# Kernel optimization log

Measured on AMD Instinct MI355X. Metric: run time of the kernel, lower is better.

Reference implementation:

```python
import jax, jax.numpy as jnp
import numpy as np

D_MODEL = 1024
NUM_HEAD = 16
D_HEAD = 64
EPS = 1e-06


def setup_inputs() -> dict:
    key = jax.random.key(0)
    ks = jax.random.split(key, 16)
    d, h = D_MODEL, 4 * D_MODEL
    s = 1.0 / np.sqrt(d)
    inp = {
        "x": jax.random.normal(ks[0], (8, 1024, d), dtype=jnp.float32),
        # LayerNorm params
        "alpha1": jnp.ones((d,), jnp.float32),
        "beta1": jnp.zeros((d,), jnp.float32),
        "alpha2": jnp.ones((d,), jnp.float32),
        "beta2": jnp.zeros((d,), jnp.float32),
        # attention projections (weights stored as [in, out])
        "w_q": jax.random.normal(ks[1], (d, d), jnp.float32) * s,
        "b_q": jnp.zeros((d,), jnp.float32),
        "w_k": jax.random.normal(ks[2], (d, d), jnp.float32) * s,
        "b_k": jnp.zeros((d,), jnp.float32),
        "w_v": jax.random.normal(ks[3], (d, d), jnp.float32) * s,
        "b_v": jnp.zeros((d,), jnp.float32),
        "w_o": jax.random.normal(ks[4], (d, d), jnp.float32) * s,
        "b_o": jnp.zeros((d,), jnp.float32),
        # MLP
        "w1": jax.random.normal(ks[5], (d, h), jnp.float32) * s,
        "b1": jnp.zeros((h,), jnp.float32),
        "w2": jax.random.normal(ks[6], (h, d), jnp.float32) * (1.0 / np.sqrt(h)),
        "b2": jnp.zeros((d,), jnp.float32),
    }
    return inp


def _layer_norm(x, alpha, beta):
    mu = jnp.mean(x, axis=-1, keepdims=True)
    # torch .var() defaults to unbiased (ddof=1) — replicate exactly
    var = jnp.var(x, axis=-1, keepdims=True, ddof=1)
    return (x - mu) / jnp.sqrt(var + EPS) * alpha + beta


def _mha(x, w_q, b_q, w_k, b_k, w_v, b_v, w_o, b_o):
    b, p, _ = x.shape
    q = (x @ w_q + b_q).reshape(b, p, NUM_HEAD, D_HEAD).transpose(0, 2, 1, 3)
    k = (x @ w_k + b_k).reshape(b, p, NUM_HEAD, D_HEAD).transpose(0, 2, 1, 3)
    v = (x @ w_v + b_v).reshape(b, p, NUM_HEAD, D_HEAD).transpose(0, 2, 1, 3)
    scores = jnp.einsum("bhqd,bhkd->bhqk", q, k) / np.sqrt(D_HEAD).astype(np.float32)
    attn = jax.nn.softmax(scores, axis=-1)
    out = jnp.einsum("bhqk,bhkd->bhqd", attn, v)
    out = out.transpose(0, 2, 1, 3).reshape(b, p, NUM_HEAD * D_HEAD)
    return out @ w_o + b_o


def reference(x, alpha1, beta1, alpha2, beta2,
              w_q, b_q, w_k, b_k, w_v, b_v, w_o, b_o,
              w1, b1, w2, b2):
    # eval mode: Dropout is identity
    x = x + _mha(_layer_norm(x, alpha1, beta1), w_q, b_q, w_k, b_k, w_v, b_v, w_o, b_o)
    h = _layer_norm(x, alpha2, beta2)
    h = jax.nn.gelu(h @ w1 + b1, approximate=False)  # nn.GELU default: exact erf
    h = h @ w2 + b2
    return x + h
```

## Files before the change

### kernel.cpp

```cpp
#include <hip/hip_runtime.h>
#include <stdint.h>

typedef float f32x4 __attribute__((ext_vector_type(4)));
typedef short s16x8 __attribute__((ext_vector_type(8)));
typedef short s16x4 __attribute__((ext_vector_type(4)));
typedef unsigned int u32x4 __attribute__((ext_vector_type(4)));

#define M_TOTAL 8192
#define DM 1024
#define HID 4096
#define SEQ 1024
#define NH 16
#define DH 64

#define BAR() __builtin_amdgcn_s_barrier()
#define LGKM0() do { asm volatile("s_waitcnt lgkmcnt(0)" ::: "memory"); __builtin_amdgcn_sched_barrier(0); } while (0)
#define VMCNT8() do { asm volatile("s_waitcnt vmcnt(8)" ::: "memory"); __builtin_amdgcn_sched_barrier(0); } while (0)
#define VMCNT0() do { asm volatile("s_waitcnt vmcnt(0)" ::: "memory"); __builtin_amdgcn_sched_barrier(0); } while (0)
#define MFMA16 __builtin_amdgcn_mfma_f32_16x16x32_bf16

__device__ __forceinline__ unsigned short f2bf(float f) {
  unsigned int u = __float_as_uint(f);
  u = (u + 0x7fffu + ((u >> 16) & 1u)) >> 16;
  return (unsigned short)u;
}

__device__ __forceinline__ void gload16(const void* g, void* l) {
  __builtin_amdgcn_global_load_lds((__attribute__((address_space(1))) void*)g,
                                   (__attribute__((address_space(3))) void*)l,
                                   16, 0, 0);
}

__device__ __forceinline__ float erf_fast(float z) {
  const float az = fabsf(z);
  const float tt = 1.0f / fmaf(0.3275911f, az, 1.0f);
  float poly = fmaf(1.061405429f, tt, -1.453152027f);
  poly = fmaf(poly, tt, 1.421413741f);
  poly = fmaf(poly, tt, -0.284496736f);
  poly = fmaf(poly, tt, 0.254829592f);
  poly *= tt;
  const float e = __expf(-az * az);
  const float r = 1.0f - poly * e;
  return (z < 0.f) ? -r : r;
}

__global__ void tcast(const float* __restrict__ W, unsigned short* __restrict__ WT,
                      int K, int N) {
  __shared__ float tile[32][33];
  const int bn = blockIdx.x, bk = blockIdx.y;
  const int tx = threadIdx.x, ty = threadIdx.y;
#pragma unroll
  for (int i = 0; i < 32; i += 8)
    tile[ty + i][tx] = W[(size_t)(bk * 32 + ty + i) * N + bn * 32 + tx];
  __syncthreads();
#pragma unroll
  for (int i = 0; i < 32; i += 8)
    WT[(size_t)(bn * 32 + ty + i) * K + bk * 32 + tx] = f2bf(tile[tx][ty + i]);
}

__global__ __launch_bounds__(256)
void vtrans(const unsigned short* __restrict__ V, unsigned short* __restrict__ VT) {
  __shared__ unsigned short tile[64][65];
  const int bh = blockIdx.y, s0 = blockIdx.x * 64;
  const int t = threadIdx.x;
  const int sr = t >> 3, c0 = (t & 7) * 8;
#pragma unroll
  for (int it = 0; it < 2; ++it) {
    const int s = it * 32 + sr;
    const s16x8 v = *(const s16x8*)(V + ((size_t)bh * SEQ + s0 + s) * DH + c0);
#pragma unroll
    for (int i = 0; i < 8; ++i) tile[c0 + i][s] = (unsigned short)v[i];
  }
  __syncthreads();
#pragma unroll
  for (int it = 0; it < 2; ++it) {
    const int d = it * 32 + sr;
    s16x8 o;
#pragma unroll
    for (int i = 0; i < 8; ++i) o[i] = (short)tile[d][c0 + i];
    *(s16x8*)(VT + ((size_t)bh * DH + d) * SEQ + s0 + c0) = o;
  }
}

__global__ __launch_bounds__(256)
void ln_kernel(const float* __restrict__ x, const float* __restrict__ alpha,
               const float* __restrict__ beta, unsigned short* __restrict__ out) {
  const int row = blockIdx.x;
  const int t = threadIdx.x;
  const int w = t >> 6, lane = t & 63;
  const float4 v = ((const float4*)(x + (size_t)row * DM))[t];

  float s = v.x + v.y + v.z + v.w;
#pragma unroll
  for (int off = 32; off; off >>= 1) s += __shfl_xor(s, off, 64);
  __shared__ float red1[4];
  __shared__ float red2[4];
  if (lane == 0) red1[w] = s;
  __syncthreads();
  const float mu = (red1[0] + red1[1] + red1[2] + red1[3]) * (1.f / 1024.f);

  const float dx = v.x - mu, dy = v.y - mu, dz = v.z - mu, dw = v.w - mu;
  float sq = dx * dx + dy * dy + dz * dz + dw * dw;
#pragma unroll
  for (int off = 32; off; off >>= 1) sq += __shfl_xor(sq, off, 64);
  if (lane == 0) red2[w] = sq;
  __syncthreads();
  const float var = (red2[0] + red2[1] + red2[2] + red2[3]) * (1.f / 1023.f);
  const float rstd = rsqrtf(var + 1e-6f);

  const float4 a = ((const float4*)alpha)[t];
  const float4 b = ((const float4*)beta)[t];
  s16x4 o;
  o[0] = (short)f2bf(dx * rstd * a.x + b.x);
  o[1] = (short)f2bf(dy * rstd * a.y + b.y);
  o[2] = (short)f2bf(dz * rstd * a.z + b.z);
  o[3] = (short)f2bf(dw * rstd * a.w + b.w);
  *(s16x4*)(out + (size_t)row * DM + 4 * t) = o;
}

template <int MODE>
__device__ __forceinline__ void epi_store(int m, int n, float v, int Nout,
                                          unsigned short* __restrict__ obf, float* of,
                                          const float* res,
                                          const float* __restrict__ bias0,
                                          const float* __restrict__ bias1,
                                          const float* __restrict__ bias2) {
  if (MODE == 0) {
    const int which = n >> 10, nn = n & 1023;
    const float* bp = (which == 0) ? bias0 : ((which == 1) ? bias1 : bias2);
    v += bp[nn];
    const int b = m >> 10, s = m & 1023, h = nn >> 6, d = nn & 63;
    obf[(size_t)which * (M_TOTAL * DM) +
        (((size_t)(b * NH + h) * SEQ + s) * DH + d)] = f2bf(v);
  } else if (MODE == 1) {
    v += bias0[n] + res[(size_t)m * Nout + n];
    of[(size_t)m * Nout + n] = v;
  } else {
    v += bias0[n];
    const float gv = 0.5f * v * (1.0f + erf_fast(v * 0.70710678118654752f));
    obf[(size_t)m * Nout + n] = f2bf(gv);
  }
}

template <int MODE>
__global__ __launch_bounds__(256, 2)
void gemmk(const unsigned short* __restrict__ A, const unsigned short* __restrict__ B,
           int K, int Nout,
           unsigned short* __restrict__ obf, float* of, const float* res,
           const float* __restrict__ bias0, const float* __restrict__ bias1,
           const float* __restrict__ bias2) {
  __shared__ __attribute__((aligned(16))) unsigned short sA[2][128 * 64];
  __shared__ __attribute__((aligned(16))) unsigned short sB[2][128 * 64];
  const int t = threadIdx.x;
  const int lane = t & 63, wid = t >> 6;
  const int g = lane >> 4, r = lane & 15;
  const int wm = wid >> 1, wn = wid & 1;

  int bid = blockIdx.y * gridDim.x + blockIdx.x;
  const int nwg = gridDim.x * gridDim.y;
  bid = (bid & 7) * (nwg >> 3) + (bid >> 3);
  const int by = bid & 63;
  const int bx = bid >> 6;
  const int m0 = by * 128, n0 = bx * 128;

  const unsigned short* Ab = A + (size_t)m0 * K;
  const unsigned short* Bb = B + (size_t)n0 * K;

  const int rb = r & 7;
  const int slot0 = (g ^ rb) * 16;
  const int slot1 = ((4 + g) ^ rb) * 16;

  f32x4 acc[4][4];
#pragma unroll
  for (int i = 0; i < 4; ++i)
#pragma unroll
    for (int j = 0; j < 4; ++j) acc[i][j] = (f32x4){0.f, 0.f, 0.f, 0.f};

  auto stage = [&](int buf, int kt) {
#pragma unroll
    for (int s2 = 0; s2 < 4; ++s2) {
      const int f = s2 * 256 + t;
      const int row = f >> 3, c = f & 7;
      const int u = c ^ (row & 7);
      gload16(Ab + (size_t)row * K + kt * 64 + u * 8, &sA[buf][(size_t)row * 64 + c * 8]);
      gload16(Bb + (size_t)row * K + kt * 64 + u * 8, &sB[buf][(size_t)row * 64 + c * 8]);
    }
  };

  const int NT = K >> 6;
  stage(0, 0);
  stage(1, (NT > 1) ? 1 : 0);
  VMCNT8();
  BAR();

  for (int tt = 0; tt < NT; ++tt) {
    const int cur = tt & 1;
    const char* sAc = (const char*)&sA[cur][0];
    const char* sBc = (const char*)&sB[cur][0];

    s16x8 av[4][2], bv[4][2];
#pragma unroll
    for (int i = 0; i < 4; ++i) {
      const int rbyte = (wm * 64 + i * 16 + r) * 128;
      av[i][0] = *(const s16x8*)(sAc + rbyte + slot0);
      av[i][1] = *(const s16x8*)(sAc + rbyte + slot1);
    }
#pragma unroll
    for (int n = 0; n < 4; ++n) {
      const int rbyte = (wn * 64 + n * 16 + r) * 128;
      bv[n][0] = *(const s16x8*)(sBc + rbyte + slot0);
      bv[n][1] = *(const s16x8*)(sBc + rbyte + slot1);
    }
    LGKM0();
    __builtin_amdgcn_s_setprio(1);
#pragma unroll
    for (int i = 0; i < 4; ++i)
#pragma unroll
      for (int n = 0; n < 4; ++n) {
        acc[i][n] = MFMA16(av[i][0], bv[n][0], acc[i][n], 0, 0, 0);
        acc[i][n] = MFMA16(av[i][1], bv[n][1], acc[i][n], 0, 0, 0);
      }
    __builtin_amdgcn_s_setprio(0);

    BAR();
    const int tp2 = (tt + 2 < NT) ? tt + 2 : NT - 1;
    stage(cur, tp2);
    VMCNT8();
    BAR();
  }

  VMCNT0();

#pragma unroll
  for (int i = 0; i < 4; ++i)
#pragma unroll
    for (int j = 0; j < 4; ++j) {
      const int m = m0 + wm * 64 + i * 16 + 4 * g + j;
#pragma unroll
      for (int nf = 0; nf < 4; ++nf) {
        const int n = n0 + wn * 64 + nf * 16 + r;
        epi_store<MODE>(m, n, acc[i][nf][j], Nout, obf, of, res, bias0, bias1, bias2);
      }
    }
}

__global__ __launch_bounds__(256)
void attn_kernel(const unsigned short* __restrict__ QKV,
                 const unsigned short* __restrict__ VT,
                 unsigned short* __restrict__ O) {
  const unsigned short* Qg = QKV;
  const unsigned short* Kg = QKV + (size_t)M_TOTAL * DM;
  const int bh = blockIdx.y;
  const int q0 = blockIdx.x * 64;
  const int t = threadIdx.x, w = t >> 6, lane = t & 63;
  const int g = lane >> 4, r = lane & 15;
  const unsigned short* Qb = Qg + (size_t)bh * SEQ * DH;
  const unsigned short* Kb = Kg + (size_t)bh * SEQ * DH;
  const unsigned short* VTb = VT + (size_t)bh * DH * SEQ;

  __shared__ __attribute__((aligned(16))) unsigned short sK[2][64 * 64];
  __shared__ __attribute__((aligned(16))) unsigned short sV[2][64 * 64];

  s16x8 qf[2];
  {
    const unsigned short* qrow = Qb + (size_t)(q0 + w * 16 + r) * DH;
    qf[0] = *(const s16x8*)(qrow + g * 8);
    qf[1] = *(const s16x8*)(qrow + 32 + g * 8);
  }

  f32x4 oacc[4];
#pragma unroll
  for (int i = 0; i < 4; ++i) oacc[i] = (f32x4){0.f, 0.f, 0.f, 0.f};
  float mrun = -1e30f, lrun = 0.f;

  auto stage = [&](int buf, int kt) {
#pragma unroll
    for (int s2 = 0; s2 < 2; ++s2) {
      const int f = s2 * 256 + t;
      const int row = f >> 3, u = (f & 7) ^ (row & 7);
      gload16(Kb + (size_t)(kt * 64 + row) * DH + u * 8, &sK[buf][f * 8]);
      gload16(VTb + (size_t)row * SEQ + kt * 64 + u * 8, &sV[buf][f * 8]);
    }
  };

  stage(0, 0);
  __syncthreads();

  for (int kt = 0; kt < SEQ / 64; ++kt) {
    const int cur = kt & 1;
    if (kt < SEQ / 64 - 1) stage(cur ^ 1, kt + 1);

    f32x4 sc[4];
#pragma unroll
    for (int nf = 0; nf < 4; ++nf) {
      sc[nf] = (f32x4){0.f, 0.f, 0.f, 0.f};
      const int rowk = nf * 16 + r;
#pragma unroll
      for (int ks = 0; ks < 2; ++ks) {
        const int u = (4 * ks + g) ^ (rowk & 7);
        const s16x8 kf = *(const s16x8*)&sK[cur][rowk * 64 + u * 8];
        sc[nf] = __builtin_amdgcn_mfma_f32_16x16x32_bf16(kf, qf[ks], sc[nf], 0, 0, 0);
      }
    }

    float pm = -1e30f;
#pragma unroll
    for (int nf = 0; nf < 4; ++nf)
#pragma unroll
      for (int j = 0; j < 4; ++j) {
        sc[nf][j] *= 0.125f;
        pm = fmaxf(pm, sc[nf][j]);
      }
    pm = fmaxf(pm, __shfl_xor(pm, 16, 64));
    pm = fmaxf(pm, __shfl_xor(pm, 32, 64));

    const float mnew = fmaxf(mrun, pm);
    const float alpha = __expf(mrun - mnew);
    mrun = mnew;

    float p[4][4];
    float ps = 0.f;
#pragma unroll
    for (int nf = 0; nf < 4; ++nf)
#pragma unroll
      for (int j = 0; j < 4; ++j) {
        p[nf][j] = __expf(sc[nf][j] - mnew);
        ps += p[nf][j];
      }
    ps += __shfl_xor(ps, 16, 64);
    ps += __shfl_xor(ps, 32, 64);
    lrun = lrun * alpha + ps;

    float ao[4];
#pragma unroll
    for (int j = 0; j < 4; ++j) ao[j] = __shfl(alpha, 4 * g + j, 64);
#pragma unroll
    for (int nf2 = 0; nf2 < 4; ++nf2)
#pragma unroll
      for (int j = 0; j < 4; ++j) oacc[nf2][j] *= ao[j];

    unsigned int pk[4][2];
#pragma unroll
    for (int nf = 0; nf < 4; ++nf)
#pragma unroll
      for (int jp = 0; jp < 2; ++jp)
        pk[nf][jp] = (unsigned int)f2bf(p[nf][2 * jp]) |
                     ((unsigned int)f2bf(p[nf][2 * jp + 1]) << 16);

    unsigned int pa32[2][4];
#pragma unroll
    for (int ks = 0; ks < 2; ++ks)
#pragma unroll
      for (int q2 = 0; q2 < 4; ++q2) {
        const int src = r + 32 * (g & 1) + 16 * (q2 >> 1);
        const unsigned int a = (unsigned int)__shfl((int)pk[2 * ks][q2 & 1], src, 64);
        const unsigned int b = (unsigned int)__shfl((int)pk[2 * ks + 1][q2 & 1], src, 64);
        pa32[ks][q2] = (g >> 1) ? b : a;
      }
    s16x8 pa[2];
#pragma unroll
    for (int ks = 0; ks < 2; ++ks) {
      u32x4 pw;
      pw[0] = pa32[ks][0]; pw[1] = pa32[ks][1];
      pw[2] = pa32[ks][2]; pw[3] = pa32[ks][3];
      pa[ks] = __builtin_bit_cast(s16x8, pw);
    }

#pragma unroll
    for (int nf2 = 0; nf2 < 4; ++nf2) {
      const int rowd = nf2 * 16 + r;
#pragma unroll
      for (int ks = 0; ks < 2; ++ks) {
        const int u = (4 * ks + g) ^ (rowd & 7);
        const s16x8 vb = *(const s16x8*)&sV[cur][rowd * 64 + u * 8];
        oacc[nf2] = __builtin_amdgcn_mfma_f32_16x16x32_bf16(pa[ks], vb, oacc[nf2], 0, 0, 0);
      }
    }
    __syncthreads();
  }

  const int b = bh >> 4, h = bh & 15;
  const float linv = 1.f / lrun;
#pragma unroll
  for (int j = 0; j < 4; ++j) {
    const float lo = __shfl(linv, 4 * g + j, 64);
    const int q = q0 + w * 16 + 4 * g + j;
    const size_t orow = ((size_t)(b * SEQ + q)) * DM + h * DH;
#pragma unroll
    for (int nf2 = 0; nf2 < 4; ++nf2)
      O[orow + nf2 * 16 + r] = f2bf(oacc[nf2][j] * lo);
  }
}

extern "C" void kernel_launch(void* const* d_in, const int* in_sizes, int n_in,
                              void* d_out, int out_size, void* d_ws, size_t ws_size,
                              hipStream_t stream) {
  const float* x   = (const float*)d_in[0];
  const float* al1 = (const float*)d_in[1];
  const float* be1 = (const float*)d_in[2];
  const float* al2 = (const float*)d_in[3];
  const float* be2 = (const float*)d_in[4];
  const float* wq  = (const float*)d_in[5];
  const float* bq  = (const float*)d_in[6];
  const float* wk  = (const float*)d_in[7];
  const float* bk  = (const float*)d_in[8];
  const float* wv  = (const float*)d_in[9];
  const float* bv  = (const float*)d_in[10];
  const float* wo  = (const float*)d_in[11];
  const float* bo  = (const float*)d_in[12];
  const float* w1  = (const float*)d_in[13];
  const float* b1  = (const float*)d_in[14];
  const float* w2  = (const float*)d_in[15];
  const float* b2  = (const float*)d_in[16];
  float* dout = (float*)d_out;

  unsigned short* ws = (unsigned short*)d_ws;
  size_t off = 0;
  auto alloc = [&](size_t n) { unsigned short* p = ws + off; off += n; return p; };
  unsigned short* WTqkv = alloc((size_t)3072 * 1024);
  unsigned short* WTo   = alloc((size_t)1024 * 1024);
  unsigned short* WT1   = alloc((size_t)4096 * 1024);
  unsigned short* WT2   = alloc((size_t)1024 * 4096);
  unsigned short* xn    = alloc((size_t)M_TOTAL * DM);
  unsigned short* QKVb  = alloc((size_t)3 * M_TOTAL * DM);
  unsigned short* VTb   = alloc((size_t)M_TOTAL * DM);
  unsigned short* attn  = alloc((size_t)M_TOTAL * DM);
  unsigned short* h1    = alloc((size_t)M_TOTAL * HID);
  (void)ws_size; (void)in_sizes; (void)n_in; (void)out_size;

  const dim3 tb(32, 8);
  tcast<<<dim3(32, 32), tb, 0, stream>>>(wq, WTqkv, 1024, 1024);
  tcast<<<dim3(32, 32), tb, 0, stream>>>(wk, WTqkv + (size_t)1024 * 1024, 1024, 1024);
  tcast<<<dim3(32, 32), tb, 0, stream>>>(wv, WTqkv + (size_t)2048 * 1024, 1024, 1024);
  tcast<<<dim3(32, 32), tb, 0, stream>>>(wo, WTo, 1024, 1024);
  tcast<<<dim3(128, 32), tb, 0, stream>>>(w1, WT1, 1024, 4096);
  tcast<<<dim3(32, 128), tb, 0, stream>>>(w2, WT2, 4096, 1024);

  ln_kernel<<<M_TOTAL, 256, 0, stream>>>(x, al1, be1, xn);
  gemmk<0><<<dim3(24, 64), 256, 0, stream>>>(xn, WTqkv, 1024, 3072,
                                             QKVb, nullptr, nullptr, bq, bk, bv);
  vtrans<<<dim3(16, 128), 256, 0, stream>>>(QKVb + 2 * (size_t)M_TOTAL * DM, VTb);
  attn_kernel<<<dim3(16, 128), 256, 0, stream>>>(QKVb, VTb, attn);
  gemmk<1><<<dim3(8, 64), 256, 0, stream>>>(attn, WTo, 1024, 1024,
                                            nullptr, dout, x, bo, nullptr, nullptr);
  ln_kernel<<<M_TOTAL, 256, 0, stream>>>(dout, al2, be2, xn);
  gemmk<2><<<dim3(32, 64), 256, 0, stream>>>(xn, WT1, 1024, 4096,
                                             h1, nullptr, nullptr, b1, nullptr, nullptr);
  gemmk<1><<<dim3(8, 64), 256, 0, stream>>>(h1, WT2, 4096, 1024,
                                            nullptr, dout, dout, b2, nullptr, nullptr);
}
```

Measured before the change: 453.6 us.

## Widen GEMM tiles to 128x256 with per-warp 64x128 output

```diff
diff --git a/kernel.cpp b/kernel.cpp
--- a/kernel.cpp
+++ b/kernel.cpp
@@ -14,8 +14,7 @@
 #define DH 64
 
 #define BAR() __builtin_amdgcn_s_barrier()
-#define LGKM0() do { asm volatile("s_waitcnt lgkmcnt(0)" ::: "memory"); __builtin_amdgcn_sched_barrier(0); } while (0)
-#define VMCNT8() do { asm volatile("s_waitcnt vmcnt(8)" ::: "memory"); __builtin_amdgcn_sched_barrier(0); } while (0)
+#define VMCNT12() do { asm volatile("s_waitcnt vmcnt(12)" ::: "memory"); __builtin_amdgcn_sched_barrier(0); } while (0)
 #define VMCNT0() do { asm volatile("s_waitcnt vmcnt(0)" ::: "memory"); __builtin_amdgcn_sched_barrier(0); } while (0)
 #define MFMA16 __builtin_amdgcn_mfma_f32_16x16x32_bf16
 
@@ -143,14 +142,14 @@
 }
 
 template <int MODE>
-__global__ __launch_bounds__(256, 2)
-void gemmk(const unsigned short* __restrict__ A, const unsigned short* __restrict__ B,
+__global__ __launch_bounds__(256, 1)
+void gemmw(const unsigned short* __restrict__ A, const unsigned short* __restrict__ B,
            int K, int Nout,
            unsigned short* __restrict__ obf, float* of, const float* res,
            const float* __restrict__ bias0, const float* __restrict__ bias1,
            const float* __restrict__ bias2) {
   __shared__ __attribute__((aligned(16))) unsigned short sA[2][128 * 64];
-  __shared__ __attribute__((aligned(16))) unsigned short sB[2][128 * 64];
+  __shared__ __attribute__((aligned(16))) unsigned short sB[2][256 * 64];
   const int t = threadIdx.x;
   const int lane = t & 63, wid = t >> 6;
   const int g = lane >> 4, r = lane & 15;
@@ -161,7 +160,7 @@
   bid = (bid & 7) * (nwg >> 3) + (bid >> 3);
   const int by = bid & 63;
   const int bx = bid >> 6;
-  const int m0 = by * 128, n0 = bx * 128;
+  const int m0 = by * 128, n0 = bx * 256;
 
   const unsigned short* Ab = A + (size_t)m0 * K;
   const unsigned short* Bb = B + (size_t)n0 * K;
@@ -170,11 +169,11 @@
   const int slot0 = (g ^ rb) * 16;
   const int slot1 = ((4 + g) ^ rb) * 16;
 
-  f32x4 acc[4][4];
+  f32x4 acc[4][8];
 #pragma unroll
   for (int i = 0; i < 4; ++i)
 #pragma unroll
-    for (int j = 0; j < 4; ++j) acc[i][j] = (f32x4){0.f, 0.f, 0.f, 0.f};
+    for (int j = 0; j < 8; ++j) acc[i][j] = (f32x4){0.f, 0.f, 0.f, 0.f};
 
   auto stage = [&](int buf, int kt) {
 #pragma unroll
@@ -183,6 +182,12 @@
       const int row = f >> 3, c = f & 7;
       const int u = c ^ (row & 7);
       gload16(Ab + (size_t)row * K + kt * 64 + u * 8, &sA[buf][(size_t)row * 64 + c * 8]);
+    }
+#pragma unroll
+    for (int s2 = 0; s2 < 8; ++s2) {
+      const int f = s2 * 256 + t;
+      const int row = f >> 3, c = f & 7;
+      const int u = c ^ (row & 7);
       gload16(Bb + (size_t)row * K + kt * 64 + u * 8, &sB[buf][(size_t)row * 64 + c * 8]);
     }
   };
@@ -190,15 +195,16 @@
   const int NT = K >> 6;
   stage(0, 0);
   stage(1, (NT > 1) ? 1 : 0);
-  VMCNT8();
+  VMCNT12();
   BAR();
+  __builtin_amdgcn_sched_barrier(0);
 
   for (int tt = 0; tt < NT; ++tt) {
     const int cur = tt & 1;
     const char* sAc = (const char*)&sA[cur][0];
     const char* sBc = (const char*)&sB[cur][0];
 
-    s16x8 av[4][2], bv[4][2];
+    s16x8 av[4][2];
 #pragma unroll
     for (int i = 0; i < 4; ++i) {
       const int rbyte = (wm * 64 + i * 16 + r) * 128;
@@ -206,27 +212,29 @@
       av[i][1] = *(const s16x8*)(sAc + rbyte + slot1);
     }
 #pragma unroll
-    for (int n = 0; n < 4; ++n) {
-      const int rbyte = (wn * 64 + n * 16 + r) * 128;
-      bv[n][0] = *(const s16x8*)(sBc + rbyte + slot0);
-      bv[n][1] = *(const s16x8*)(sBc + rbyte + slot1);
-    }
-    LGKM0();
-    __builtin_amdgcn_s_setprio(1);
-#pragma unroll
-    for (int i = 0; i < 4; ++i)
-#pragma unroll
-      for (int n = 0; n < 4; ++n) {
-        acc[i][n] = MFMA16(av[i][0], bv[n][0], acc[i][n], 0, 0, 0);
-        acc[i][n] = MFMA16(av[i][1], bv[n][1], acc[i][n], 0, 0, 0);
-      }
-    __builtin_amdgcn_s_setprio(0);
+    for (int nh = 0; nh < 2; ++nh) {
+      s16x8 bv[4][2];
+#pragma unroll
+      for (int nf = 0; nf < 4; ++nf) {
+        const int rbyte = (wn * 128 + nh * 64 + nf * 16 + r) * 128;
+        bv[nf][0] = *(const s16x8*)(sBc + rbyte + slot0);
+        bv[nf][1] = *(const s16x8*)(sBc + rbyte + slot1);
+      }
+#pragma unroll
+      for (int i = 0; i < 4; ++i)
+#pragma unroll
+        for (int nf = 0; nf < 4; ++nf) {
+          acc[i][nh * 4 + nf] = MFMA16(av[i][0], bv[nf][0], acc[i][nh * 4 + nf], 0, 0, 0);
+          acc[i][nh * 4 + nf] = MFMA16(av[i][1], bv[nf][1], acc[i][nh * 4 + nf], 0, 0, 0);
+        }
+    }
 
     BAR();
     const int tp2 = (tt + 2 < NT) ? tt + 2 : NT - 1;
     stage(cur, tp2);
-    VMCNT8();
+    VMCNT12();
     BAR();
+    __builtin_amdgcn_sched_barrier(0);
   }
 
   VMCNT0();
@@ -237,8 +245,8 @@
     for (int j = 0; j < 4; ++j) {
       const int m = m0 + wm * 64 + i * 16 + 4 * g + j;
 #pragma unroll
-      for (int nf = 0; nf < 4; ++nf) {
-        const int n = n0 + wn * 64 + nf * 16 + r;
+      for (int nf = 0; nf < 8; ++nf) {
+        const int n = n0 + wn * 128 + nf * 16 + r;
         epi_store<MODE>(m, n, acc[i][nf][j], Nout, obf, of, res, bias0, bias1, bias2);
       }
     }
@@ -437,15 +445,15 @@
   tcast<<<dim3(32, 128), tb, 0, stream>>>(w2, WT2, 4096, 1024);
 
   ln_kernel<<<M_TOTAL, 256, 0, stream>>>(x, al1, be1, xn);
-  gemmk<0><<<dim3(24, 64), 256, 0, stream>>>(xn, WTqkv, 1024, 3072,
+  gemmw<0><<<dim3(12, 64), 256, 0, stream>>>(xn, WTqkv, 1024, 3072,
                                              QKVb, nullptr, nullptr, bq, bk, bv);
   vtrans<<<dim3(16, 128), 256, 0, stream>>>(QKVb + 2 * (size_t)M_TOTAL * DM, VTb);
   attn_kernel<<<dim3(16, 128), 256, 0, stream>>>(QKVb, VTb, attn);
-  gemmk<1><<<dim3(8, 64), 256, 0, stream>>>(attn, WTo, 1024, 1024,
+  gemmw<1><<<dim3(4, 64), 256, 0, stream>>>(attn, WTo, 1024, 1024,
                                             nullptr, dout, x, bo, nullptr, nullptr);
   ln_kernel<<<M_TOTAL, 256, 0, stream>>>(dout, al2, be2, xn);
-  gemmk<2><<<dim3(32, 64), 256, 0, stream>>>(xn, WT1, 1024, 4096,
+  gemmw<2><<<dim3(16, 64), 256, 0, stream>>>(xn, WT1, 1024, 4096,
                                              h1, nullptr, nullptr, b1, nullptr, nullptr);
-  gemmk<1><<<dim3(8, 64), 256, 0, stream>>>(h1, WT2, 4096, 1024,
+  gemmw<1><<<dim3(4, 64), 256, 0, stream>>>(h1, WT2, 4096, 1024,
                                             nullptr, dout, dout, b2, nullptr, nullptr);
 }
```

Result: slower. 594.5 us (+31.1%).
